# Kernel optimization log

Measured on AMD Instinct MI355X. Metric: run time of the kernel, lower is better.

The kernel has to match this reference:

```python
import jax, jax.numpy as jnp
import numpy as np

IN_DIM = 64  # in_dim, single head (num_heads=1)
SCALE = IN_DIM ** -0.5


def setup_inputs() -> dict:
    key = jax.random.key(0)
    k1, k2, k3 = jax.random.split(key, 3)
    B, N, C = 8, 3136, 147
    x = jax.random.normal(k1, (B, N, C), dtype=jnp.float32)
    # Linear weights stored pre-transposed: y = x @ W (+ b)
    W_qkv = jax.random.normal(k2, (C, 3 * IN_DIM), dtype=jnp.float32) * (C ** -0.5)
    W_proj = jax.random.normal(k3, (IN_DIM, IN_DIM), dtype=jnp.float32) * (IN_DIM ** -0.5)
    b_proj = jnp.zeros((IN_DIM,), dtype=jnp.float32)
    return {"x": x, "W_qkv": W_qkv, "W_proj": W_proj, "b_proj": b_proj}


def reference(x, W_qkv, W_proj, b_proj):
    B, N, C = x.shape
    qkv = (x @ W_qkv).reshape(B, N, 3, IN_DIM)  # [B, N, 3, D]
    q = qkv[:, :, 0]  # [B, N, D] (num_heads == 1)
    k = qkv[:, :, 1]
    v = qkv[:, :, 2]
    attn = jax.nn.softmax(jnp.einsum('bqd,bkd->bqk', q, k) * SCALE, axis=-1)  # [B, N, N]
    out = jnp.einsum('bqk,bkd->bqd', attn, v)  # [B, N, D]
    out = out @ W_proj + b_proj
    return v + out  # v-residual
```

## Files before the change

### kernel.cpp

```cpp
#include <hip/hip_runtime.h>

typedef short  bhalf8   __attribute__((ext_vector_type(8)));
typedef float  floatx16 __attribute__((ext_vector_type(16)));
typedef float  float4e  __attribute__((ext_vector_type(4)));

#define NTOK 3136
#define CDIM 147
#define NQT  98
#define KVT  49
#define NCHUNK 8
#define QTB8 13
#define PARTB 4352

static __device__ __forceinline__ unsigned short f2bf(float f) {
    unsigned u = __float_as_uint(f);
    u += 0x7fffu + ((u >> 16) & 1u);
    return (unsigned short)(u >> 16);
}
static __device__ __forceinline__ float bf2f(unsigned short h) {
    return __uint_as_float(((unsigned)h) << 16);
}
static __device__ __forceinline__ unsigned packbf2(float a, float b) {
    unsigned r;
    asm("v_cvt_pk_bf16_f32 %0, %1, %2" : "=v"(r) : "v"(a), "v"(b));
    return r;
}
static __device__ __forceinline__ float fexp2(float x) {
#if __has_builtin(__builtin_amdgcn_exp2f)
    return __builtin_amdgcn_exp2f(x);
#else
    return __expf(x * 0.69314718056f);
#endif
}

__global__ __launch_bounds__(256) void prep_w_kernel(
    const float* __restrict__ W, unsigned short* __restrict__ WbT)
{
    const int idx = blockIdx.x * 256 + threadIdx.x;
    if (idx >= 192 * 160) return;
    const int c = idx / 160, k = idx - c * 160;
    WbT[idx] = (k < CDIM) ? f2bf(W[(size_t)k * 192 + c]) : (unsigned short)0;
}

__global__ __launch_bounds__(384) void qkv_mfma_kernel(
    const float* __restrict__ x, const unsigned short* __restrict__ WbT,
    unsigned short* __restrict__ qb, unsigned short* __restrict__ kb,
    unsigned short* __restrict__ vT)
{
    __shared__ __align__(16) unsigned char xls[32 * 384];
    const int tid = threadIdx.x;
    const int wave = tid >> 6, lane = tid & 63;
    const int l31 = lane & 31, hi = lane >> 5;
    const int n0g = blockIdx.x * 32;
    const int b = n0g / NTOK, nn0 = n0g - b * NTOK;
    const float SM = 0.125f * 1.44269504f;

    for (int i = tid; i < 640; i += 384) {
        const int row = i / 20, c = i - row * 20;
        const float* src = x + (size_t)(n0g + row) * CDIM + c * 8;
        float f[8];
        if (c < 18) {
            const float4e a = *reinterpret_cast<const float4e*>(src);
            const float4e v2 = *reinterpret_cast<const float4e*>(src + 4);
            f[0]=a[0]; f[1]=a[1]; f[2]=a[2]; f[3]=a[3];
            f[4]=v2[0]; f[5]=v2[1]; f[6]=v2[2]; f[7]=v2[3];
        } else if (c == 18) {
            f[0]=src[0]; f[1]=src[1]; f[2]=src[2];
            f[3]=f[4]=f[5]=f[6]=f[7]=0.f;
        } else {
            f[0]=f[1]=f[2]=f[3]=f[4]=f[5]=f[6]=f[7]=0.f;
        }
        uint4 u;
        u.x = packbf2(f[0], f[1]); u.y = packbf2(f[2], f[3]);
        u.z = packbf2(f[4], f[5]); u.w = packbf2(f[6], f[7]);
        const int phys = (c & ~7) | ((c & 7) ^ (row & 7));
        *reinterpret_cast<uint4*>(&xls[row * 384 + phys * 16]) = u;
    }
    __syncthreads();

    const int wcol = wave * 32;
    const bhalf8* wrow = reinterpret_cast<const bhalf8*>(WbT + (size_t)(wcol + l31) * 160);
    floatx16 acc;
#pragma unroll
    for (int r = 0; r < 16; ++r) acc[r] = 0.f;

    if (wave < 4) {
#pragma unroll
        for (int s = 0; s < 10; ++s) {
            const int slot = 2 * s + hi;
            const int phys = (slot & ~7) | ((slot & 7) ^ (l31 & 7));
            const bhalf8 xf = *reinterpret_cast<const bhalf8*>(&xls[l31 * 384 + phys * 16]);
            acc = __builtin_amdgcn_mfma_f32_32x32x16_bf16(xf, wrow[slot], acc, 0, 0, 0);
        }
        unsigned short* dst = (wave < 2) ? qb : kb;
        const float scl = (wave < 2) ? SM : 1.0f;
        const int c0 = (wave & 1) * 32 + l31;
#pragma unroll
        for (int r = 0; r < 16; ++r) {
            const int n = n0g + (r & 3) + 8 * (r >> 2) + 4 * hi;
            dst[(size_t)n * 64 + c0] = f2bf(acc[r] * scl);
        }
    } else {
#pragma unroll
        for (int s = 0; s < 10; ++s) {
            const int slot = 2 * s + hi;
            const int phys = (slot & ~7) | ((slot & 7) ^ (l31 & 7));
            const bhalf8 xf = *reinterpret_cast<const bhalf8*>(&xls[l31 * 384 + phys * 16]);
            acc = __builtin_amdgcn_mfma_f32_32x32x16_bf16(wrow[slot], xf, acc, 0, 0, 0);
        }
        const int nc = nn0 + l31;
#pragma unroll
        for (int r = 0; r < 16; ++r) {
            const int c = (wave - 4) * 32 + (r & 3) + 8 * (r >> 2) + 4 * hi;
            vT[((size_t)b * 64 + c) * NTOK + nc] = f2bf(acc[r]);
        }
    }
}

static __device__ __forceinline__ bhalf8 build_frag(unsigned a0, unsigned a1,
                                                    unsigned a2, unsigned a3, int hi)
{
    const unsigned py1 = __shfl_xor(hi ? a0 : a2, 32);
    const unsigned py2 = __shfl_xor(hi ? a1 : a3, 32);
    union { unsigned w[4]; bhalf8 v; } f;
    f.w[0] = hi ? py1 : a0;
    f.w[1] = hi ? py2 : a1;
    f.w[2] = hi ? a2 : py1;
    f.w[3] = hi ? a3 : py2;
    return f.v;
}

static __device__ __forceinline__ void attn_epilogue(
    const floatx16& accO0, const floatx16& accO1, float inv,
    const float* __restrict__ Wp, const float* __restrict__ bp,
    const unsigned short* __restrict__ vb, float* __restrict__ orow,
    int q, int l31, int hi)
{
    unsigned ok0[8], ok1[8];
#pragma unroll
    for (int w = 0; w < 8; ++w) {
        ok0[w] = packbf2(accO0[2 * w] * inv, accO0[2 * w + 1] * inv);
        ok1[w] = packbf2(accO1[2 * w] * inv, accO1[2 * w + 1] * inv);
    }
    floatx16 accP0, accP1;
#pragma unroll
    for (int r = 0; r < 16; ++r) { accP0[r] = 0.f; accP1[r] = 0.f; }
#pragma unroll
    for (int ks = 0; ks < 4; ++ks) {
        const int t = ks & 1;
        const bhalf8 of = (ks >> 1) ? build_frag(ok1[4*t], ok1[4*t+1], ok1[4*t+2], ok1[4*t+3], hi)
                                    : build_frag(ok0[4*t], ok0[4*t+1], ok0[4*t+2], ok0[4*t+3], hi);
        union { unsigned w[4]; bhalf8 v; } wa, wb;
#pragma unroll
        for (int jj = 0; jj < 4; ++jj) {
            const int d0 = 16 * ks + 8 * hi + 2 * jj;
            wa.w[jj] = packbf2(Wp[(size_t)d0 * 64 + l31],      Wp[(size_t)(d0 + 1) * 64 + l31]);
            wb.w[jj] = packbf2(Wp[(size_t)d0 * 64 + 32 + l31], Wp[(size_t)(d0 + 1) * 64 + 32 + l31]);
        }
        accP0 = __builtin_amdgcn_mfma_f32_32x32x16_bf16(wa.v, of, accP0, 0, 0, 0);
        accP1 = __builtin_amdgcn_mfma_f32_32x32x16_bf16(wb.v, of, accP1, 0, 0, 0);
    }
#pragma unroll
    for (int r = 0; r < 16; ++r) {
        const int e0 = (r & 3) + 8 * (r >> 2) + 4 * hi;
        const int e1 = e0 + 32;
        const float va = bf2f(vb[(size_t)e0 * NTOK + q]);
        const float vc = bf2f(vb[(size_t)e1 * NTOK + q]);
        orow[(size_t)q * 64 + e0] = accP0[r] + bp[e0] + va;
        orow[(size_t)q * 64 + e1] = accP1[r] + bp[e1] + vc;
    }
}

__global__ __launch_bounds__(512) void attn_split_kernel(
    const unsigned short* __restrict__ qb,
    const unsigned short* __restrict__ kbf,
    const unsigned short* __restrict__ vT,
    char* __restrict__ part)
{
    __shared__ __align__(16) unsigned char lds[2][16384];
    const int tid  = threadIdx.x;
    const int wave = tid >> 6, lane = tid & 63;
    const int l31 = lane & 31, hi = lane >> 5;
    const int qtb = blockIdx.x, b = blockIdx.y, ck = blockIdx.z;
    int qt = qtb * 8 + wave; if (qt >= NQT) qt = NQT - 1;
    const size_t bofs = (size_t)b * NTOK * 64;
    const int q0 = qt * 32;

    const bhalf8* qrow = reinterpret_cast<const bhalf8*>(qb + bofs + (size_t)(q0 + l31) * 64);
    bhalf8 Qf[4];
#pragma unroll
    for (int s = 0; s < 4; ++s) Qf[s] = qrow[2 * s + hi];

    floatx16 accO0, accO1, z16;
#pragma unroll
    for (int r = 0; r < 16; ++r) { accO0[r] = 0.f; accO1[r] = 0.f; z16[r] = 0.f; }
    float lsum = 0.f;

    const unsigned short* vb = vT + (size_t)b * 64 * NTOK;
    const int kv_lo = (ck * KVT) / NCHUNK;
    const int kv_hi = ((ck + 1) * KVT) / NCHUNK;

    const int r0 = tid >> 3,  s0i = tid & 7;
    const int swz0 = (s0i ^ (r0 & 7)) << 4;
    uint4 rK, rV;

#define STAGE_LOAD(kvt_) do {                                                   \
        rK = reinterpret_cast<const uint4*>(                                    \
            kbf + bofs + (size_t)(kvt_) * 64 * 64)[tid];                        \
        rV = *reinterpret_cast<const uint4*>(                                   \
            vb + (size_t)r0 * NTOK + (kvt_) * 64 + s0i * 8);                    \
    } while (0)

#define STAGE_WRITE(buf_) do {                                                  \
        *reinterpret_cast<uint4*>(&lds[buf_][r0 * 128 + swz0])        = rK;     \
        *reinterpret_cast<uint4*>(&lds[buf_][8192 + r0 * 128 + swz0]) = rV;     \
    } while (0)

    STAGE_LOAD(kv_lo);
    int buf = 0;
    const int kswz = (l31 & 7);
    for (int kvt = kv_lo; kvt < kv_hi; ++kvt) {
        STAGE_WRITE(buf);
        if (kvt + 1 < kv_hi) STAGE_LOAD(kvt + 1);
        __syncthreads();

        floatx16 s0, s1;
        {
            const int sl = (hi ^ kswz) << 4;
            const bhalf8 kf0 = *reinterpret_cast<const bhalf8*>(&lds[buf][l31 * 128 + sl]);
            const bhalf8 kf1 = *reinterpret_cast<const bhalf8*>(&lds[buf][(32 + l31) * 128 + sl]);
            s0 = __builtin_amdgcn_mfma_f32_32x32x16_bf16(kf0, Qf[0], z16, 0, 0, 0);
            s1 = __builtin_amdgcn_mfma_f32_32x32x16_bf16(kf1, Qf[0], z16, 0, 0, 0);
        }
#pragma unroll
        for (int s = 1; s < 4; ++s) {
            const int sl = ((2 * s + hi) ^ kswz) << 4;
            const bhalf8 kf0 = *reinterpret_cast<const bhalf8*>(&lds[buf][l31 * 128 + sl]);
            const bhalf8 kf1 = *reinterpret_cast<const bhalf8*>(&lds[buf][(32 + l31) * 128 + sl]);
            s0 = __builtin_amdgcn_mfma_f32_32x32x16_bf16(kf0, Qf[s], s0, 0, 0, 0);
            s1 = __builtin_amdgcn_mfma_f32_32x32x16_bf16(kf1, Qf[s], s1, 0, 0, 0);
        }
        float ps0 = 0.f, ps1 = 0.f;
#pragma unroll
        for (int r = 0; r < 16; ++r) {
            const float p0 = fexp2(s0[r]); s0[r] = p0;
            const float p1 = fexp2(s1[r]); s1[r] = p1;
            ps0 += p0; ps1 += p1;
        }
        lsum += ps0 + ps1;
        unsigned pk0[8], pk1[8];
#pragma unroll
        for (int w = 0; w < 8; ++w) {
            pk0[w] = packbf2(s0[2 * w], s0[2 * w + 1]);
            pk1[w] = packbf2(s1[2 * w], s1[2 * w + 1]);
        }
#pragma unroll
        for (int u = 0; u < 2; ++u) {
#pragma unroll
            for (int t = 0; t < 2; ++t) {
                const bhalf8 pf = u ? build_frag(pk1[4*t], pk1[4*t+1], pk1[4*t+2], pk1[4*t+3], hi)
                                    : build_frag(pk0[4*t], pk0[4*t+1], pk0[4*t+2], pk0[4*t+3], hi);
                const int sl = ((4 * u + 2 * t + hi) ^ kswz) << 4;
                const bhalf8 v0 = *reinterpret_cast<const bhalf8*>(&lds[buf][8192 + l31 * 128 + sl]);
                const bhalf8 v1 = *reinterpret_cast<const bhalf8*>(&lds[buf][8192 + (32 + l31) * 128 + sl]);
                accO0 = __builtin_amdgcn_mfma_f32_32x32x16_bf16(v0, pf, accO0, 0, 0, 0);
                accO1 = __builtin_amdgcn_mfma_f32_32x32x16_bf16(v1, pf, accO1, 0, 0, 0);
            }
        }
        buf ^= 1;
    }
#undef STAGE_LOAD
#undef STAGE_WRITE

    char* pbb = part + ((size_t)(b * NQT + qt) * NCHUNK + ck) * PARTB;
#pragma unroll
    for (int rg = 0; rg < 4; ++rg) {
        uint2 w0, w1;
        w0.x = packbf2(accO0[4*rg],     accO0[4*rg + 1]);
        w0.y = packbf2(accO0[4*rg + 2], accO0[4*rg + 3]);
        w1.x = packbf2(accO1[4*rg],     accO1[4*rg + 1]);
        w1.y = packbf2(accO1[4*rg + 2], accO1[4*rg + 3]);
        *reinterpret_cast<uint2*>(pbb + (rg * 64 + lane) * 8)        = w0;
        *reinterpret_cast<uint2*>(pbb + 2048 + (rg * 64 + lane) * 8) = w1;
    }
    *reinterpret_cast<float*>(pbb + 4096 + lane * 4) = lsum;
}

__global__ __launch_bounds__(256) void attn_combine_kernel(
    const char* __restrict__ part,
    const unsigned short* __restrict__ vT,
    const float* __restrict__ Wp, const float* __restrict__ bp,
    float* __restrict__ out)
{
    const int wid  = blockIdx.x * 4 + (threadIdx.x >> 6);
    const int lane = threadIdx.x & 63;
    const int qt   = wid % NQT;
    const int b    = wid / NQT;
    const int l31 = lane & 31, hi = lane >> 5;
    const char* pbase = part + (size_t)(b * NQT + qt) * NCHUNK * PARTB;

    floatx16 accO0, accO1;
#pragma unroll
    for (int r = 0; r < 16; ++r) { accO0[r] = 0.f; accO1[r] = 0.f; }
    float lsum = 0.f;
#pragma unroll
    for (int c = 0; c < NCHUNK; ++c) {
        const char* pbb = pbase + (size_t)c * PARTB;
#pragma unroll
        for (int rg = 0; rg < 4; ++rg) {
            const uint2 u0 = *reinterpret_cast<const uint2*>(pbb + (rg * 64 + lane) * 8);
            const uint2 u1 = *reinterpret_cast<const uint2*>(pbb + 2048 + (rg * 64 + lane) * 8);
            accO0[4*rg]     += __uint_as_float(u0.x << 16);
            accO0[4*rg + 1] += __uint_as_float(u0.x & 0xffff0000u);
            accO0[4*rg + 2] += __uint_as_float(u0.y << 16);
            accO0[4*rg + 3] += __uint_as_float(u0.y & 0xffff0000u);
            accO1[4*rg]     += __uint_as_float(u1.x << 16);
            accO1[4*rg + 1] += __uint_as_float(u1.x & 0xffff0000u);
            accO1[4*rg + 2] += __uint_as_float(u1.y << 16);
            accO1[4*rg + 3] += __uint_as_float(u1.y & 0xffff0000u);
        }
        lsum += *reinterpret_cast<const float*>(pbb + 4096 + lane * 4);
    }
    const float L = lsum + __shfl_xor(lsum, 32);
    const unsigned short* vb = vT + (size_t)b * 64 * NTOK;
    attn_epilogue(accO0, accO1, 1.0f / L, Wp, bp, vb, out + (size_t)b * NTOK * 64,
                  qt * 32 + l31, l31, hi);
}

__global__ __launch_bounds__(64) void attn_kernel(
    const unsigned short* __restrict__ qb,
    const unsigned short* __restrict__ kbf,
    const unsigned short* __restrict__ vT,
    const float* __restrict__ Wp, const float* __restrict__ bp,
    float* __restrict__ out)
{
    const int qt = blockIdx.x, b = blockIdx.y;
    const int lane = threadIdx.x;
    const int l31 = lane & 31, hi = lane >> 5;
    const size_t bofs = (size_t)b * NTOK * 64;
    const int q0 = qt * 32;

    const bhalf8* qrow = reinterpret_cast<const bhalf8*>(qb + bofs + (size_t)(q0 + l31) * 64);
    bhalf8 Qf[4];
#pragma unroll
    for (int s = 0; s < 4; ++s) Qf[s] = qrow[2 * s + hi];

    floatx16 accO0, accO1;
#pragma unroll
    for (int r = 0; r < 16; ++r) { accO0[r] = 0.f; accO1[r] = 0.f; }
    float lsum = 0.f;
    const unsigned short* vb = vT + (size_t)b * 64 * NTOK;
    for (int kvt = 0; kvt < KVT; ++kvt) {
        const int kv0 = kvt * 64;
        const bhalf8* kr0 = reinterpret_cast<const bhalf8*>(kbf + bofs + (size_t)(kv0 + l31) * 64);
        const bhalf8* kr1 = reinterpret_cast<const bhalf8*>(kbf + bofs + (size_t)(kv0 + 32 + l31) * 64);
        floatx16 s0, s1;
#pragma unroll
        for (int r = 0; r < 16; ++r) { s0[r] = 0.f; s1[r] = 0.f; }
#pragma unroll
        for (int s = 0; s < 4; ++s) {
            s0 = __builtin_amdgcn_mfma_f32_32x32x16_bf16(kr0[2 * s + hi], Qf[s], s0, 0, 0, 0);
            s1 = __builtin_amdgcn_mfma_f32_32x32x16_bf16(kr1[2 * s + hi], Qf[s], s1, 0, 0, 0);
        }
        float ps0 = 0.f, ps1 = 0.f;
#pragma unroll
        for (int r = 0; r < 16; ++r) {
            const float p0 = fexp2(s0[r]); s0[r] = p0;
            const float p1 = fexp2(s1[r]); s1[r] = p1;
            ps0 += p0; ps1 += p1;
        }
        lsum += ps0 + ps1;
        unsigned pk0[8], pk1[8];
#pragma unroll
        for (int w = 0; w < 8; ++w) {
            pk0[w] = packbf2(s0[2 * w], s0[2 * w + 1]);
            pk1[w] = packbf2(s1[2 * w], s1[2 * w + 1]);
        }
#pragma unroll
        for (int u = 0; u < 2; ++u) {
#pragma unroll
            for (int t = 0; t < 2; ++t) {
                const bhalf8 pf = u ? build_frag(pk1[4*t], pk1[4*t+1], pk1[4*t+2], pk1[4*t+3], hi)
                                    : build_frag(pk0[4*t], pk0[4*t+1], pk0[4*t+2], pk0[4*t+3], hi);
                const int col = kv0 + 32 * u + 16 * t + 8 * hi;
                const bhalf8 v0 = *reinterpret_cast<const bhalf8*>(vb + (size_t)l31 * NTOK + col);
                const bhalf8 v1 = *reinterpret_cast<const bhalf8*>(vb + (size_t)(32 + l31) * NTOK + col);
                accO0 = __builtin_amdgcn_mfma_f32_32x32x16_bf16(v0, pf, accO0, 0, 0, 0);
                accO1 = __builtin_amdgcn_mfma_f32_32x32x16_bf16(v1, pf, accO1, 0, 0, 0);
            }
        }
    }
    const float L = lsum + __shfl_xor(lsum, 32);
    attn_epilogue(accO0, accO1, 1.0f / L, Wp, bp, vb, out + bofs,
                  q0 + l31, l31, hi);
}

extern "C" void kernel_launch(void* const* d_in, const int* in_sizes, int n_in,
                              void* d_out, int out_size, void* d_ws, size_t ws_size,
                              hipStream_t stream)
{
    const float* x  = (const float*)d_in[0];
    const float* Wq = (const float*)d_in[1];
    const float* Wp = (const float*)d_in[2];
    const float* bp = (const float*)d_in[3];
    float* out = (float*)d_out;

    unsigned short* qbuf = (unsigned short*)d_ws;
    unsigned short* kbuf = qbuf + (size_t)8 * NTOK * 64;
    unsigned short* vTb  = kbuf + (size_t)8 * NTOK * 64;
    const size_t bf_bytes = (size_t)3 * 8 * NTOK * 64 * 2;
    char* part = (char*)d_ws + bf_bytes;
    const size_t part_bytes = (size_t)8 * NQT * NCHUNK * PARTB;
    unsigned short* WbT = (unsigned short*)((char*)d_ws + bf_bytes + part_bytes);
    const size_t need = bf_bytes + part_bytes + 192 * 160 * 2;

    if (ws_size >= need) {
        prep_w_kernel<<<dim3(120), 256, 0, stream>>>(Wq, WbT);
        qkv_mfma_kernel<<<dim3(8 * NTOK / 32), 384, 0, stream>>>(x, WbT, qbuf, kbuf, vTb);
        attn_split_kernel<<<dim3(QTB8, 8, NCHUNK), 512, 0, stream>>>(qbuf, kbuf, vTb, part);
        attn_combine_kernel<<<dim3(8 * NQT / 4), 256, 0, stream>>>(part, vTb, Wp, bp, out);
    } else {
        prep_w_kernel<<<dim3(120), 256, 0, stream>>>(Wq, (unsigned short*)part);
        qkv_mfma_kernel<<<dim3(8 * NTOK / 32), 384, 0, stream>>>(x, (unsigned short*)part, qbuf, kbuf, vTb);
        attn_kernel<<<dim3(NQT, 8), 64, 0, stream>>>(qbuf, kbuf, vTb, Wp, bp, out);
    }
}
```

Before: 60.61 us.

## Fuse split-KV combine into attention kernel via last-arriver atomic counter

The separate combine kernel is removed. Each split-KV wave publishes its partial output with atomic stores and a release fence, then increments a per-query-tile counter; the last of the eight chunks reduces all partials and runs the projection and residual epilogue. This saves a kernel launch and the gap between kernels, but the tail now does serialized combine work and relies on the flags being zeroed in the prep kernel. s_setprio hints are also added around the MFMA sections to favour matrix issue over other waves.

Measured after the change: 155.1 us. +155.9%, slower.

```diff
diff --git a/kernel.cpp b/kernel.cpp
--- a/kernel.cpp
+++ b/kernel.cpp
@@ -34,9 +34,11 @@
 }
 
 __global__ __launch_bounds__(256) void prep_w_kernel(
-    const float* __restrict__ W, unsigned short* __restrict__ WbT)
+    const float* __restrict__ W, unsigned short* __restrict__ WbT,
+    int* __restrict__ flags)
 {
     const int idx = blockIdx.x * 256 + threadIdx.x;
+    if (flags && idx < 8 * NQT) flags[idx] = 0;
     if (idx >= 192 * 160) return;
     const int c = idx / 160, k = idx - c * 160;
     WbT[idx] = (k < CDIM) ? f2bf(W[(size_t)k * 192 + c]) : (unsigned short)0;
@@ -175,14 +177,17 @@
     const unsigned short* __restrict__ qb,
     const unsigned short* __restrict__ kbf,
     const unsigned short* __restrict__ vT,
-    char* __restrict__ part)
+    char* __restrict__ part, int* __restrict__ flags,
+    const float* __restrict__ Wp, const float* __restrict__ bp,
+    float* __restrict__ out)
 {
     __shared__ __align__(16) unsigned char lds[2][16384];
     const int tid  = threadIdx.x;
     const int wave = tid >> 6, lane = tid & 63;
     const int l31 = lane & 31, hi = lane >> 5;
     const int qtb = blockIdx.x, b = blockIdx.y, ck = blockIdx.z;
-    int qt = qtb * 8 + wave; if (qt >= NQT) qt = NQT - 1;
+    const int qtid = qtb * 8 + wave;
+    const int qt = (qtid < NQT) ? qtid : NQT - 1;
     const size_t bofs = (size_t)b * NTOK * 64;
     const int q0 = qt * 32;
 
@@ -225,6 +230,7 @@
         __syncthreads();
 
         floatx16 s0, s1;
+        __builtin_amdgcn_s_setprio(1);
         {
             const int sl = (hi ^ kswz) << 4;
             const bhalf8 kf0 = *reinterpret_cast<const bhalf8*>(&lds[buf][l31 * 128 + sl]);
@@ -240,6 +246,7 @@
             s0 = __builtin_amdgcn_mfma_f32_32x32x16_bf16(kf0, Qf[s], s0, 0, 0, 0);
             s1 = __builtin_amdgcn_mfma_f32_32x32x16_bf16(kf1, Qf[s], s1, 0, 0, 0);
         }
+        __builtin_amdgcn_s_setprio(0);
         float ps0 = 0.f, ps1 = 0.f;
 #pragma unroll
         for (int r = 0; r < 16; ++r) {
@@ -254,6 +261,7 @@
             pk0[w] = packbf2(s0[2 * w], s0[2 * w + 1]);
             pk1[w] = packbf2(s1[2 * w], s1[2 * w + 1]);
         }
+        __builtin_amdgcn_s_setprio(1);
 #pragma unroll
         for (int u = 0; u < 2; ++u) {
 #pragma unroll
@@ -267,64 +275,68 @@
                 accO1 = __builtin_amdgcn_mfma_f32_32x32x16_bf16(v1, pf, accO1, 0, 0, 0);
             }
         }
+        __builtin_amdgcn_s_setprio(0);
         buf ^= 1;
     }
 #undef STAGE_LOAD
 #undef STAGE_WRITE
 
+    if (qtid >= NQT) return;
+
     char* pbb = part + ((size_t)(b * NQT + qt) * NCHUNK + ck) * PARTB;
 #pragma unroll
     for (int rg = 0; rg < 4; ++rg) {
-        uint2 w0, w1;
-        w0.x = packbf2(accO0[4*rg],     accO0[4*rg + 1]);
-        w0.y = packbf2(accO0[4*rg + 2], accO0[4*rg + 3]);
-        w1.x = packbf2(accO1[4*rg],     accO1[4*rg + 1]);
-        w1.y = packbf2(accO1[4*rg + 2], accO1[4*rg + 3]);
-        *reinterpret_cast<uint2*>(pbb + (rg * 64 + lane) * 8)        = w0;
-        *reinterpret_cast<uint2*>(pbb + 2048 + (rg * 64 + lane) * 8) = w1;
-    }
-    *reinterpret_cast<float*>(pbb + 4096 + lane * 4) = lsum;
-}
-
-__global__ __launch_bounds__(256) void attn_combine_kernel(
-    const char* __restrict__ part,
-    const unsigned short* __restrict__ vT,
-    const float* __restrict__ Wp, const float* __restrict__ bp,
-    float* __restrict__ out)
-{
-    const int wid  = blockIdx.x * 4 + (threadIdx.x >> 6);
-    const int lane = threadIdx.x & 63;
-    const int qt   = wid % NQT;
-    const int b    = wid / NQT;
-    const int l31 = lane & 31, hi = lane >> 5;
+        const unsigned long long w0 =
+            (unsigned long long)packbf2(accO0[4*rg], accO0[4*rg+1]) |
+            ((unsigned long long)packbf2(accO0[4*rg+2], accO0[4*rg+3]) << 32);
+        const unsigned long long w1 =
+            (unsigned long long)packbf2(accO1[4*rg], accO1[4*rg+1]) |
+            ((unsigned long long)packbf2(accO1[4*rg+2], accO1[4*rg+3]) << 32);
+        __hip_atomic_store((unsigned long long*)(pbb + (rg * 64 + lane) * 8), w0,
+                           __ATOMIC_RELAXED, __HIP_MEMORY_SCOPE_AGENT);
+        __hip_atomic_store((unsigned long long*)(pbb + 2048 + (rg * 64 + lane) * 8), w1,
+                           __ATOMIC_RELAXED, __HIP_MEMORY_SCOPE_AGENT);
+    }
+    __hip_atomic_store((float*)(pbb + 4096 + lane * 4), lsum,
+                       __ATOMIC_RELAXED, __HIP_MEMORY_SCOPE_AGENT);
+
+    __builtin_amdgcn_fence(__ATOMIC_RELEASE, "agent");
+    int old = 0;
+    if (lane == 0)
+        old = __hip_atomic_fetch_add(&flags[b * NQT + qt], 1,
+                                     __ATOMIC_RELAXED, __HIP_MEMORY_SCOPE_AGENT);
+    old = __shfl(old, 0);
+    if (old != NCHUNK - 1) return;
+
+    __builtin_amdgcn_fence(__ATOMIC_ACQUIRE, "agent");
     const char* pbase = part + (size_t)(b * NQT + qt) * NCHUNK * PARTB;
-
-    floatx16 accO0, accO1;
-#pragma unroll
-    for (int r = 0; r < 16; ++r) { accO0[r] = 0.f; accO1[r] = 0.f; }
-    float lsum = 0.f;
+    floatx16 cO0, cO1;
+#pragma unroll
+    for (int r = 0; r < 16; ++r) { cO0[r] = 0.f; cO1[r] = 0.f; }
+    float ltot = 0.f;
 #pragma unroll
     for (int c = 0; c < NCHUNK; ++c) {
-        const char* pbb = pbase + (size_t)c * PARTB;
+        const char* pc = pbase + (size_t)c * PARTB;
 #pragma unroll
         for (int rg = 0; rg < 4; ++rg) {
-            const uint2 u0 = *reinterpret_cast<const uint2*>(pbb + (rg * 64 + lane) * 8);
-            const uint2 u1 = *reinterpret_cast<const uint2*>(pbb + 2048 + (rg * 64 + lane) * 8);
-            accO0[4*rg]     += __uint_as_float(u0.x << 16);
-            accO0[4*rg + 1] += __uint_as_float(u0.x & 0xffff0000u);
-            accO0[4*rg + 2] += __uint_as_float(u0.y << 16);
-            accO0[4*rg + 3] += __uint_as_float(u0.y & 0xffff0000u);
-            accO1[4*rg]     += __uint_as_float(u1.x << 16);
-            accO1[4*rg + 1] += __uint_as_float(u1.x & 0xffff0000u);
-            accO1[4*rg + 2] += __uint_as_float(u1.y << 16);
-            accO1[4*rg + 3] += __uint_as_float(u1.y & 0xffff0000u);
-        }
-        lsum += *reinterpret_cast<const float*>(pbb + 4096 + lane * 4);
-    }
-    const float L = lsum + __shfl_xor(lsum, 32);
-    const unsigned short* vb = vT + (size_t)b * 64 * NTOK;
-    attn_epilogue(accO0, accO1, 1.0f / L, Wp, bp, vb, out + (size_t)b * NTOK * 64,
-                  qt * 32 + l31, l31, hi);
+            const uint2 u0 = *reinterpret_cast<const uint2*>(pc + (rg * 64 + lane) * 8);
+            const uint2 u1 = *reinterpret_cast<const uint2*>(pc + 2048 + (rg * 64 + lane) * 8);
+            cO0[4*rg]     += __uint_as_float(u0.x << 16);
+            cO0[4*rg + 1] += __uint_as_float(u0.x & 0xffff0000u);
+            cO0[4*rg + 2] += __uint_as_float(u0.y << 16);
+            cO0[4*rg + 3] += __uint_as_float(u0.y & 0xffff0000u);
+            cO1[4*rg]     += __uint_as_float(u1.x << 16);
+            cO1[4*rg + 1] += __uint_as_float(u1.x & 0xffff0000u);
+            cO1[4*rg + 2] += __uint_as_float(u1.y << 16);
+            cO1[4*rg + 3] += __uint_as_float(u1.y & 0xffff0000u);
+        }
+        ltot += *reinterpret_cast<const float*>(pc + 4096 + lane * 4);
+    }
+    const float L = ltot + __shfl_xor(ltot, 32);
+    attn_epilogue(cO0, cO1, 1.0f / L, Wp, bp, vb, out + bofs, q0 + l31, l31, hi);
+    if (lane == 0)
+        __hip_atomic_store(&flags[b * NQT + qt], 0,
+                           __ATOMIC_RELAXED, __HIP_MEMORY_SCOPE_AGENT);
 }
 
 __global__ __launch_bounds__(64) void attn_kernel(
@@ -412,15 +424,16 @@
     char* part = (char*)d_ws + bf_bytes;
     const size_t part_bytes = (size_t)8 * NQT * NCHUNK * PARTB;
     unsigned short* WbT = (unsigned short*)((char*)d_ws + bf_bytes + part_bytes);
-    const size_t need = bf_bytes + part_bytes + 192 * 160 * 2;
+    int* flags = (int*)((char*)d_ws + bf_bytes + part_bytes + 192 * 160 * 2);
+    const size_t need = bf_bytes + part_bytes + 192 * 160 * 2 + 8 * NQT * 4;
 
     if (ws_size >= need) {
-        prep_w_kernel<<<dim3(120), 256, 0, stream>>>(Wq, WbT);
+        prep_w_kernel<<<dim3(120), 256, 0, stream>>>(Wq, WbT, flags);
         qkv_mfma_kernel<<<dim3(8 * NTOK / 32), 384, 0, stream>>>(x, WbT, qbuf, kbuf, vTb);
-        attn_split_kernel<<<dim3(QTB8, 8, NCHUNK), 512, 0, stream>>>(qbuf, kbuf, vTb, part);
-        attn_combine_kernel<<<dim3(8 * NQT / 4), 256, 0, stream>>>(part, vTb, Wp, bp, out);
+        attn_split_kernel<<<dim3(QTB8, 8, NCHUNK), 512, 0, stream>>>(
+            qbuf, kbuf, vTb, part, flags, Wp, bp, out);
     } else {
-        prep_w_kernel<<<dim3(120), 256, 0, stream>>>(Wq, (unsigned short*)part);
+        prep_w_kernel<<<dim3(120), 256, 0, stream>>>(Wq, (unsigned short*)part, nullptr);
         qkv_mfma_kernel<<<dim3(8 * NTOK / 32), 384, 0, stream>>>(x, (unsigned short*)part, qbuf, kbuf, vTb);
         attn_kernel<<<dim3(NQT, 8), 64, 0, stream>>>(qbuf, kbuf, vTb, Wp, bp, out);
     }
```

## Process two KV tiles per iteration with a single 32KB LDS stage

Applied to the files above, without the earlier changes.

Replaces the per-tile double-buffered LDS pipeline with one 32KB buffer that holds two 64-row K/V tiles. Each thread now loads two 16-byte pieces per matrix, and both tiles are consumed in one loop iteration. The two QK^T/softmax chains in an iteration are independent, which gives the scheduler more MFMA and exp work to interleave between barriers. The trade-off is that global prefetch is only issued after the barrier, and a trailing barrier is added so the buffer can be reused. On odd-length chunks the prefetch may also read a tile past the chunk end, which can run past the end of the K buffer for the last batch.

New measurement: 68.51 us. 13.0% more time.

```diff
diff --git a/kernel.cpp b/kernel.cpp
--- a/kernel.cpp
+++ b/kernel.cpp
@@ -177,7 +177,7 @@
     const unsigned short* __restrict__ vT,
     char* __restrict__ part)
 {
-    __shared__ __align__(16) unsigned char lds[2][16384];
+    __shared__ __align__(16) unsigned char lds[32768];
     const int tid  = threadIdx.x;
     const int wave = tid >> 6, lane = tid & 63;
     const int l31 = lane & 31, hi = lane >> 5;
@@ -200,77 +200,122 @@
     const int kv_lo = (ck * KVT) / NCHUNK;
     const int kv_hi = ((ck + 1) * KVT) / NCHUNK;
 
-    const int r0 = tid >> 3,  s0i = tid & 7;
-    const int swz0 = (s0i ^ (r0 & 7)) << 4;
-    uint4 rK, rV;
-
-#define STAGE_LOAD(kvt_) do {                                                   \
-        rK = reinterpret_cast<const uint4*>(                                    \
-            kbf + bofs + (size_t)(kvt_) * 64 * 64)[tid];                        \
-        rV = *reinterpret_cast<const uint4*>(                                   \
-            vb + (size_t)r0 * NTOK + (kvt_) * 64 + s0i * 8);                    \
+    const int rK = tid >> 2, sK = tid & 3;
+    const int tV = tid >> 8;
+    const int rV = (tid >> 2) & 63, sV = tid & 3;
+    uint4 rk0, rk1, rv0, rv1;
+
+#define STAGE_LOAD(base_) do {                                                  \
+        const unsigned short* kp = kbf + bofs + (size_t)((base_) * 64 + rK) * 64;\
+        rk0 = *reinterpret_cast<const uint4*>(kp + sK * 8);                     \
+        rk1 = *reinterpret_cast<const uint4*>(kp + (sK + 4) * 8);               \
+        const unsigned short* vp = vb + (size_t)rV * NTOK + (base_) * 64 + tV * 64;\
+        rv0 = *reinterpret_cast<const uint4*>(vp + sV * 8);                     \
+        rv1 = *reinterpret_cast<const uint4*>(vp + (sV + 4) * 8);               \
     } while (0)
 
-#define STAGE_WRITE(buf_) do {                                                  \
-        *reinterpret_cast<uint4*>(&lds[buf_][r0 * 128 + swz0])        = rK;     \
-        *reinterpret_cast<uint4*>(&lds[buf_][8192 + r0 * 128 + swz0]) = rV;     \
+#define STAGE_WRITE() do {                                                      \
+        *reinterpret_cast<uint4*>(&lds[rK * 128 + ((sK ^ (rK & 7)) << 4)])      = rk0; \
+        *reinterpret_cast<uint4*>(&lds[rK * 128 + (((sK + 4) ^ (rK & 7)) << 4)])= rk1; \
+        *reinterpret_cast<uint4*>(&lds[16384 + tV * 8192 + rV * 128 + ((sV ^ (rV & 7)) << 4)])       = rv0; \
+        *reinterpret_cast<uint4*>(&lds[16384 + tV * 8192 + rV * 128 + (((sV + 4) ^ (rV & 7)) << 4)]) = rv1; \
     } while (0)
 
+#define LDK(row_, sl_) (*reinterpret_cast<const bhalf8*>(&lds[(row_) * 128 + (sl_)]))
+#define LDV(t_, row_, sl_) (*reinterpret_cast<const bhalf8*>(&lds[16384 + (t_) * 8192 + (row_) * 128 + (sl_)]))
+
+    const int kswz = l31 & 7;
     STAGE_LOAD(kv_lo);
-    int buf = 0;
-    const int kswz = (l31 & 7);
-    for (int kvt = kv_lo; kvt < kv_hi; ++kvt) {
-        STAGE_WRITE(buf);
-        if (kvt + 1 < kv_hi) STAGE_LOAD(kvt + 1);
+    for (int base = kv_lo; base < kv_hi; base += 2) {
+        STAGE_WRITE();
         __syncthreads();
-
-        floatx16 s0, s1;
+        if (base + 2 < kv_hi) STAGE_LOAD(base + 2);
+        const bool two = (base + 1 < kv_hi);
+
+        floatx16 sA0, sA1;
         {
             const int sl = (hi ^ kswz) << 4;
-            const bhalf8 kf0 = *reinterpret_cast<const bhalf8*>(&lds[buf][l31 * 128 + sl]);
-            const bhalf8 kf1 = *reinterpret_cast<const bhalf8*>(&lds[buf][(32 + l31) * 128 + sl]);
-            s0 = __builtin_amdgcn_mfma_f32_32x32x16_bf16(kf0, Qf[0], z16, 0, 0, 0);
-            s1 = __builtin_amdgcn_mfma_f32_32x32x16_bf16(kf1, Qf[0], z16, 0, 0, 0);
+            sA0 = __builtin_amdgcn_mfma_f32_32x32x16_bf16(LDK(l31, sl),      Qf[0], z16, 0, 0, 0);
+            sA1 = __builtin_amdgcn_mfma_f32_32x32x16_bf16(LDK(32 + l31, sl), Qf[0], z16, 0, 0, 0);
         }
 #pragma unroll
         for (int s = 1; s < 4; ++s) {
             const int sl = ((2 * s + hi) ^ kswz) << 4;
-            const bhalf8 kf0 = *reinterpret_cast<const bhalf8*>(&lds[buf][l31 * 128 + sl]);
-            const bhalf8 kf1 = *reinterpret_cast<const bhalf8*>(&lds[buf][(32 + l31) * 128 + sl]);
-            s0 = __builtin_amdgcn_mfma_f32_32x32x16_bf16(kf0, Qf[s], s0, 0, 0, 0);
-            s1 = __builtin_amdgcn_mfma_f32_32x32x16_bf16(kf1, Qf[s], s1, 0, 0, 0);
-        }
-        float ps0 = 0.f, ps1 = 0.f;
+            sA0 = __builtin_amdgcn_mfma_f32_32x32x16_bf16(LDK(l31, sl),      Qf[s], sA0, 0, 0, 0);
+            sA1 = __builtin_amdgcn_mfma_f32_32x32x16_bf16(LDK(32 + l31, sl), Qf[s], sA1, 0, 0, 0);
+        }
+        float psA = 0.f;
 #pragma unroll
         for (int r = 0; r < 16; ++r) {
-            const float p0 = fexp2(s0[r]); s0[r] = p0;
-            const float p1 = fexp2(s1[r]); s1[r] = p1;
-            ps0 += p0; ps1 += p1;
-        }
-        lsum += ps0 + ps1;
-        unsigned pk0[8], pk1[8];
+            const float p0 = fexp2(sA0[r]); sA0[r] = p0;
+            const float p1 = fexp2(sA1[r]); sA1[r] = p1;
+            psA += p0 + p1;
+        }
+        lsum += psA;
+        unsigned pkA0[8], pkA1[8];
 #pragma unroll
         for (int w = 0; w < 8; ++w) {
-            pk0[w] = packbf2(s0[2 * w], s0[2 * w + 1]);
-            pk1[w] = packbf2(s1[2 * w], s1[2 * w + 1]);
+            pkA0[w] = packbf2(sA0[2 * w], sA0[2 * w + 1]);
+            pkA1[w] = packbf2(sA1[2 * w], sA1[2 * w + 1]);
+        }
+        unsigned pkB0[8], pkB1[8];
+        if (two) {
+            floatx16 sB0, sB1;
+            {
+                const int sl = (hi ^ kswz) << 4;
+                sB0 = __builtin_amdgcn_mfma_f32_32x32x16_bf16(LDK(64 + l31, sl), Qf[0], z16, 0, 0, 0);
+                sB1 = __builtin_amdgcn_mfma_f32_32x32x16_bf16(LDK(96 + l31, sl), Qf[0], z16, 0, 0, 0);
+            }
+#pragma unroll
+            for (int s = 1; s < 4; ++s) {
+                const int sl = ((2 * s + hi) ^ kswz) << 4;
+                sB0 = __builtin_amdgcn_mfma_f32_32x32x16_bf16(LDK(64 + l31, sl), Qf[s], sB0, 0, 0, 0);
+                sB1 = __builtin_amdgcn_mfma_f32_32x32x16_bf16(LDK(96 + l31, sl), Qf[s], sB1, 0, 0, 0);
+            }
+            float psB = 0.f;
+#pragma unroll
+            for (int r = 0; r < 16; ++r) {
+                const float p0 = fexp2(sB0[r]); sB0[r] = p0;
+                const float p1 = fexp2(sB1[r]); sB1[r] = p1;
+                psB += p0 + p1;
+            }
+            lsum += psB;
+#pragma unroll
+            for (int w = 0; w < 8; ++w) {
+                pkB0[w] = packbf2(sB0[2 * w], sB0[2 * w + 1]);
+                pkB1[w] = packbf2(sB1[2 * w], sB1[2 * w + 1]);
+            }
         }
 #pragma unroll
         for (int u = 0; u < 2; ++u) {
 #pragma unroll
-            for (int t = 0; t < 2; ++t) {
-                const bhalf8 pf = u ? build_frag(pk1[4*t], pk1[4*t+1], pk1[4*t+2], pk1[4*t+3], hi)
-                                    : build_frag(pk0[4*t], pk0[4*t+1], pk0[4*t+2], pk0[4*t+3], hi);
-                const int sl = ((4 * u + 2 * t + hi) ^ kswz) << 4;
-                const bhalf8 v0 = *reinterpret_cast<const bhalf8*>(&lds[buf][8192 + l31 * 128 + sl]);
-                const bhalf8 v1 = *reinterpret_cast<const bhalf8*>(&lds[buf][8192 + (32 + l31) * 128 + sl]);
-                accO0 = __builtin_amdgcn_mfma_f32_32x32x16_bf16(v0, pf, accO0, 0, 0, 0);
-                accO1 = __builtin_amdgcn_mfma_f32_32x32x16_bf16(v1, pf, accO1, 0, 0, 0);
-            }
-        }
-        buf ^= 1;
+            for (int t2 = 0; t2 < 2; ++t2) {
+                const bhalf8 pf = u ? build_frag(pkA1[4*t2], pkA1[4*t2+1], pkA1[4*t2+2], pkA1[4*t2+3], hi)
+                                    : build_frag(pkA0[4*t2], pkA0[4*t2+1], pkA0[4*t2+2], pkA0[4*t2+3], hi);
+                const int sl = ((4 * u + 2 * t2 + hi) ^ kswz) << 4;
+                accO0 = __builtin_amdgcn_mfma_f32_32x32x16_bf16(LDV(0, l31, sl),      pf, accO0, 0, 0, 0);
+                accO1 = __builtin_amdgcn_mfma_f32_32x32x16_bf16(LDV(0, 32 + l31, sl), pf, accO1, 0, 0, 0);
+            }
+        }
+        if (two) {
+#pragma unroll
+            for (int u = 0; u < 2; ++u) {
+#pragma unroll
+                for (int t2 = 0; t2 < 2; ++t2) {
+                    const bhalf8 pf = u ? build_frag(pkB1[4*t2], pkB1[4*t2+1], pkB1[4*t2+2], pkB1[4*t2+3], hi)
+                                        : build_frag(pkB0[4*t2], pkB0[4*t2+1], pkB0[4*t2+2], pkB0[4*t2+3], hi);
+                    const int sl = ((4 * u + 2 * t2 + hi) ^ kswz) << 4;
+                    accO0 = __builtin_amdgcn_mfma_f32_32x32x16_bf16(LDV(1, l31, sl),      pf, accO0, 0, 0, 0);
+                    accO1 = __builtin_amdgcn_mfma_f32_32x32x16_bf16(LDV(1, 32 + l31, sl), pf, accO1, 0, 0, 0);
+                }
+            }
+        }
+        __syncthreads();
     }
 #undef STAGE_LOAD
 #undef STAGE_WRITE
+#undef LDK
+#undef LDV
 
     char* pbb = part + ((size_t)(b * NQT + qt) * NCHUNK + ck) * PARTB;
 #pragma unroll
```
